# Performance work log

Measured on AMD Instinct MI355X. Metric: run time of the kernel, lower is better.

The kernel has to match this reference:

```python
import jax, jax.numpy as jnp
import numpy as np

H = 128          # hidden_dim
L = 3            # n_layers
G = 128          # num graphs in batch
BN_EPS = 1e-5


def setup_inputs() -> dict:
    key = jax.random.key(0)
    ks = jax.random.split(key, 16)
    N, E, ND, ED = 2048, 8192, 32, 16
    s = lambda k, shape, fan: jax.random.normal(k, shape, dtype=jnp.float32) / np.sqrt(fan)
    return {
        "x": jax.random.normal(ks[0], (N, ND), dtype=jnp.float32),
        "edge_index": jax.random.randint(ks[1], (2, E), 0, N),
        "edge_attr": jax.random.normal(ks[2], (E, ED), dtype=jnp.float32),
        "batch": jnp.sort(jax.random.randint(ks[3], (N,), 0, G)),
        "node_W": s(ks[4], (ND, H), ND),
        "node_b": jnp.zeros((H,), jnp.float32),
        "edge_W": s(ks[5], (L, ED, H * H), ED),
        "edge_b": jnp.zeros((L, H * H), jnp.float32),
        "root_W": s(ks[6], (L, H, H), H),
        "conv_bias": jnp.zeros((L, H), jnp.float32),
        "bn_gamma": jnp.ones((L, H), jnp.float32),
        "bn_beta": jnp.zeros((L, H), jnp.float32),
        "cls_W1": s(ks[7], (H, 64), H),
        "cls_b1": jnp.zeros((64,), jnp.float32),
        "cls_W2": s(ks[8], (64, 1), 64),
        "cls_b2": jnp.zeros((1,), jnp.float32),
    }


def _segment_mean(vals, ids, num_segments):
    ssum = jax.ops.segment_sum(vals, ids, num_segments=num_segments)
    cnt = jax.ops.segment_sum(jnp.ones((vals.shape[0],), vals.dtype), ids,
                              num_segments=num_segments)
    return ssum / jnp.maximum(cnt, 1.0)[:, None]


def reference(x, edge_index, edge_attr, batch, node_W, node_b, edge_W, edge_b,
              root_W, conv_bias, bn_gamma, bn_beta, cls_W1, cls_b1, cls_W2, cls_b2):
    N = x.shape[0]
    src, dst = edge_index[0], edge_index[1]
    h = x @ node_W + node_b                                   # [N, H]
    for l in range(L):
        # edge-conditioned weights: [E, H, H]
        W = (edge_attr @ edge_W[l] + edge_b[l]).reshape(-1, H, H)
        msg = jnp.einsum('ei,eio->eo', h[src], W)             # gather + per-edge matmul
        agg = _segment_mean(msg, dst, N)                      # scatter-mean
        x_new = h @ root_W[l] + agg + conv_bias[l]
        # BatchNorm (batch statistics, training-mode math)
        mu = jnp.mean(x_new, axis=0)
        var = jnp.var(x_new, axis=0)
        x_new = (x_new - mu) * jax.lax.rsqrt(var + BN_EPS) * bn_gamma[l] + bn_beta[l]
        x_new = jax.nn.relu(x_new)                            # dropout omitted (eval)
        h = h + x_new                                         # residual
    g = _segment_mean(h, batch, G)                            # global mean pool [G, H]
    out = jax.nn.relu(g @ cls_W1 + cls_b1) @ cls_W2 + cls_b2  # classifier
    return out.squeeze(-1)                                    # [G]
```

## Files before the change

kernel.cpp:

```cpp
#include <hip/hip_runtime.h>
#include <cstddef>
#include <cstdint>

#define H 128
#define EDIM 16
#define NLAYER 3
#define NSLICE 18
#define WCOLS (NSLICE * H)
#define TM 64
#define TN 64
#define TK 16

typedef unsigned short ushort_t;
typedef unsigned int uint_t;
typedef __attribute__((ext_vector_type(8))) short bf16x8;
typedef __attribute__((ext_vector_type(4))) float f32x4;

__device__ __forceinline__ ushort_t f2bf(float f) {
    uint_t u = __builtin_bit_cast(uint_t, f);
    u += 0x7fffu + ((u >> 16) & 1u);
    return (ushort_t)(u >> 16);
}

__global__ __launch_bounds__(256) void gemm_bsliced(
    const float* __restrict__ A, const float* __restrict__ B,
    const float* __restrict__ bias, float* __restrict__ C,
    ushort_t* __restrict__ Cbf, int M, int K, int N)
{
    __shared__ float As[TK][TM + 4];
    __shared__ float Bs[TK][TN + 4];
    const int bm = blockIdx.y * TM;
    const int bn = blockIdx.x * TN;
    const int tid = threadIdx.x;
    const int tx = tid & 15;
    const int ty = tid >> 4;

    float acc[4][4];
#pragma unroll
    for (int i = 0; i < 4; ++i)
#pragma unroll
        for (int j = 0; j < 4; ++j) acc[i][j] = 0.f;

    const int ka = tid & 15, ma = tid >> 4;
    const int nb = tid & 63, kb = tid >> 6;

    for (int k0 = 0; k0 < K; k0 += TK) {
#pragma unroll
        for (int r = 0; r < 4; ++r)
            As[ka][ma + 16 * r] = A[(size_t)(bm + ma + 16 * r) * K + (k0 + ka)];
#pragma unroll
        for (int r = 0; r < 4; ++r)
            Bs[kb + 4 * r][nb] = B[(size_t)(k0 + kb + 4 * r) * N + bn + nb];
        __syncthreads();
#pragma unroll
        for (int kk = 0; kk < TK; ++kk) {
            const float4 a4 = *(const float4*)&As[kk][ty * 4];
            const float4 b4 = *(const float4*)&Bs[kk][tx * 4];
            const float a[4] = {a4.x, a4.y, a4.z, a4.w};
            const float b[4] = {b4.x, b4.y, b4.z, b4.w};
#pragma unroll
            for (int i = 0; i < 4; ++i)
#pragma unroll
                for (int j = 0; j < 4; ++j)
                    acc[i][j] = fmaf(a[i], b[j], acc[i][j]);
        }
        __syncthreads();
    }

#pragma unroll
    for (int i = 0; i < 4; ++i) {
        const int row = bm + ty * 4 + i;
        float4 v;
        v.x = acc[i][0] + bias[(bn + tx * 4 + 0) & 127];
        v.y = acc[i][1] + bias[(bn + tx * 4 + 1) & 127];
        v.z = acc[i][2] + bias[(bn + tx * 4 + 2) & 127];
        v.w = acc[i][3] + bias[(bn + tx * 4 + 3) & 127];
        *(float4*)&C[(size_t)row * N + bn + tx * 4] = v;
        if (Cbf) {
            ushort_t* o = &Cbf[(size_t)row * N + bn + tx * 4];
            o[0] = f2bf(v.x); o[1] = f2bf(v.y); o[2] = f2bf(v.z); o[3] = f2bf(v.w);
        }
    }
}

__global__ __launch_bounds__(256) void prep_weights(
    const float* __restrict__ eW, const float* __restrict__ eb,
    const float* __restrict__ rW, ushort_t* __restrict__ Wt)
{
    __shared__ ushort_t tile[128][136];
    const int b = blockIdx.x;
    const int l = b / NSLICE, s = b % NSLICE;
    const float* S = (s < 16) ? (eW + ((size_t)l * 16 + s) * (H * H))
                   : (s == 16 ? (eb + (size_t)l * H * H)
                              : (rW + (size_t)l * H * H));
    const int t = threadIdx.x;
    const int k = t >> 1, o0 = (t & 1) * 64;
#pragma unroll
    for (int j = 0; j < 64; j += 4) {
        float4 v = *(const float4*)&S[(size_t)k * H + o0 + j];
        tile[k][o0 + j + 0] = f2bf(v.x);
        tile[k][o0 + j + 1] = f2bf(v.y);
        tile[k][o0 + j + 2] = f2bf(v.z);
        tile[k][o0 + j + 3] = f2bf(v.w);
    }
    __syncthreads();
    const int n = t >> 1, k0 = (t & 1) * 64;
    ushort_t* out = Wt + ((size_t)l * WCOLS + s * H + n) * H + k0;
#pragma unroll 8
    for (int j = 0; j < 64; ++j) out[j] = tile[k0 + j][n];
}

__global__ __launch_bounds__(256) void mfma_gemm(
    const ushort_t* __restrict__ hbf, const ushort_t* __restrict__ Wt,
    float* __restrict__ C)
{
    __shared__ ushort_t As[64][136];
    __shared__ ushort_t Bs[64][136];
    const int tid = threadIdx.x;
    const int v0 = blockIdx.y * 64;
    const int n0 = blockIdx.x * 64;

    {
        const int row = tid >> 2, col0 = (tid & 3) * 32;
        const ushort_t* ga = hbf + (size_t)(v0 + row) * H + col0;
        const ushort_t* gb = Wt + (size_t)(n0 + row) * H + col0;
#pragma unroll
        for (int j = 0; j < 32; j += 8) {
            *(uint4*)&As[row][col0 + j] = *(const uint4*)(ga + j);
            *(uint4*)&Bs[row][col0 + j] = *(const uint4*)(gb + j);
        }
    }
    __syncthreads();

    const int wave = tid >> 6, lane = tid & 63;
    const int l15 = lane & 15, kg = lane >> 4;
    const int mrow = wave * 16 + l15;

    f32x4 acc0 = {0.f, 0.f, 0.f, 0.f};
    f32x4 acc1 = {0.f, 0.f, 0.f, 0.f};
    f32x4 acc2 = {0.f, 0.f, 0.f, 0.f};
    f32x4 acc3 = {0.f, 0.f, 0.f, 0.f};

#pragma unroll
    for (int s = 0; s < 4; ++s) {
        const int k = s * 32 + kg * 8;
        bf16x8 a = *(const bf16x8*)&As[mrow][k];
        bf16x8 b0 = *(const bf16x8*)&Bs[0 * 16 + l15][k];
        bf16x8 b1 = *(const bf16x8*)&Bs[1 * 16 + l15][k];
        bf16x8 b2 = *(const bf16x8*)&Bs[2 * 16 + l15][k];
        bf16x8 b3 = *(const bf16x8*)&Bs[3 * 16 + l15][k];
        acc0 = __builtin_amdgcn_mfma_f32_16x16x32_bf16(a, b0, acc0, 0, 0, 0);
        acc1 = __builtin_amdgcn_mfma_f32_16x16x32_bf16(a, b1, acc1, 0, 0, 0);
        acc2 = __builtin_amdgcn_mfma_f32_16x16x32_bf16(a, b2, acc2, 0, 0, 0);
        acc3 = __builtin_amdgcn_mfma_f32_16x16x32_bf16(a, b3, acc3, 0, 0, 0);
    }

    const size_t base = (size_t)(v0 + wave * 16 + kg * 4) * WCOLS + n0 + l15;
#pragma unroll
    for (int r = 0; r < 4; ++r) {
        C[base + (size_t)r * WCOLS + 0]  = acc0[r];
        C[base + (size_t)r * WCOLS + 16] = acc1[r];
        C[base + (size_t)r * WCOLS + 32] = acc2[r];
        C[base + (size_t)r * WCOLS + 48] = acc3[r];
    }
}

__global__ void count_kernel(const int* __restrict__ dst, const int* __restrict__ batch,
                             float* cntN, float* cntG, int E, int N)
{
    int t = blockIdx.x * 256 + threadIdx.x;
    if (t < E) atomicAdd(&cntN[dst[t]], 1.f);
    if (t < N) atomicAdd(&cntG[batch[t]], 1.f);
}

__global__ __launch_bounds__(256) void edge_combine(
    const float* __restrict__ Pbuf, const float* __restrict__ ea,
    const int* __restrict__ src, const int* __restrict__ dst,
    float* __restrict__ agg, int E)
{
    const int e = blockIdx.x * 2 + (threadIdx.x >> 7);
    const int o = threadIdx.x & 127;
    if (e >= E) return;
    const int s = src[e], d = dst[e];
    const float* Pe = Pbuf + (size_t)s * WCOLS;
    float m = Pe[16 * H + o];
#pragma unroll
    for (int dd = 0; dd < EDIM; ++dd)
        m = fmaf(ea[e * EDIM + dd], Pe[dd * H + o], m);
    atomicAdd(&agg[d * H + o], m);
}

__global__ __launch_bounds__(256) void stats_kernel(
    const float* __restrict__ Pbuf, const float* __restrict__ agg,
    const float* __restrict__ cnt, const float* __restrict__ conv_b,
    float* __restrict__ xnew, float* __restrict__ bnS, float* __restrict__ bnQ)
{
    __shared__ float s1[H], s2[H];
    const int c = threadIdx.x & 127;
    const int half = threadIdx.x >> 7;
    const int row0 = blockIdx.x * 32;
    const float cb = conv_b[c];
    float s = 0.f, q = 0.f;
    for (int r = half; r < 32; r += 2) {
        const int v = row0 + r;
        const float rc = 1.0f / fmaxf(cnt[v], 1.0f);
        const float val = Pbuf[(size_t)v * WCOLS + 17 * H + c] + cb
                        + agg[v * H + c] * rc;
        xnew[v * H + c] = val;
        s += val;
        q += val * val;
    }
    if (half == 1) { s1[c] = s; s2[c] = q; }
    __syncthreads();
    if (half == 0) {
        atomicAdd(&bnS[c], s + s1[c]);
        atomicAdd(&bnQ[c], q + s2[c]);
    }
}

__global__ __launch_bounds__(256) void bn_apply(
    float* __restrict__ h, ushort_t* __restrict__ hbf,
    const float* __restrict__ xnew,
    const float* __restrict__ bnS, const float* __restrict__ bnQ,
    const float* __restrict__ gamma, const float* __restrict__ beta,
    const int* __restrict__ batch, float* __restrict__ gsum, int N, int last)
{
    const int idx = blockIdx.x * 256 + threadIdx.x;
    const int c = idx & 127;
    const int v = idx >> 7;
    const float invN = 1.0f / (float)N;
    const float mu = bnS[c] * invN;
    const float var = bnQ[c] * invN - mu * mu;
    const float val = (xnew[idx] - mu) * rsqrtf(var + 1e-5f) * gamma[c] + beta[c];
    const float hn = h[idx] + fmaxf(val, 0.f);
    h[idx] = hn;
    hbf[idx] = f2bf(hn);
    if (last) atomicAdd(&gsum[batch[v] * H + c], hn);
}

__global__ void classifier_kernel(
    const float* __restrict__ gsum, const float* __restrict__ cntG,
    const float* __restrict__ W1, const float* __restrict__ b1,
    const float* __restrict__ W2, const float* __restrict__ b2,
    float* __restrict__ out)
{
    const int g = blockIdx.x;
    const int j = threadIdx.x;
    const float rc = 1.0f / fmaxf(cntG[g], 1.0f);
    float acc = b1[j];
#pragma unroll 8
    for (int i = 0; i < H; ++i)
        acc = fmaf(gsum[g * H + i] * rc, W1[i * 64 + j], acc);
    float pv = fmaxf(acc, 0.f) * W2[j];
#pragma unroll
    for (int off = 32; off > 0; off >>= 1)
        pv += __shfl_down(pv, off);
    if (j == 0) out[g] = pv + b2[0];
}

extern "C" void kernel_launch(void* const* d_in, const int* in_sizes, int n_in,
                              void* d_out, int out_size, void* d_ws, size_t ws_size,
                              hipStream_t stream)
{
    const float* x      = (const float*)d_in[0];
    const int*   eidx   = (const int*)  d_in[1];
    const float* eattr  = (const float*)d_in[2];
    const int*   batch  = (const int*)  d_in[3];
    const float* node_W = (const float*)d_in[4];
    const float* node_b = (const float*)d_in[5];
    const float* edge_W = (const float*)d_in[6];
    const float* edge_b = (const float*)d_in[7];
    const float* root_W = (const float*)d_in[8];
    const float* conv_b = (const float*)d_in[9];
    const float* gamma  = (const float*)d_in[10];
    const float* beta   = (const float*)d_in[11];
    const float* W1     = (const float*)d_in[12];
    const float* b1     = (const float*)d_in[13];
    const float* W2     = (const float*)d_in[14];
    const float* b2     = (const float*)d_in[15];
    float* out = (float*)d_out;

    const int N = in_sizes[0] / 32;
    const int E = in_sizes[1] / 2;
    const int G = out_size;

    float* ws = (float*)d_ws;
    float* agg  = ws;
    float* cntN = agg  + (size_t)3 * N * H;
    float* cntG = cntN + N;
    float* bnS  = cntG + G;
    float* bnQ  = bnS  + NLAYER * H;
    float* gsum = bnQ  + NLAYER * H;
    float* h    = gsum + (size_t)G * H;
    float* xnew = h    + (size_t)N * H;
    ushort_t* hbf = (ushort_t*)(xnew + (size_t)N * H);
    ushort_t* Wt  = hbf + (size_t)N * H;
    float* Pbuf = (float*)(Wt + (size_t)NLAYER * WCOLS * H);

    const size_t zf = (size_t)3 * N * H + N + G + 2 * NLAYER * H + (size_t)G * H;
    hipMemsetAsync(agg, 0, zf * sizeof(float), stream);

    const int* src = eidx;
    const int* dst = eidx + E;

    const int tmax = (E > N ? E : N);
    count_kernel<<<(tmax + 255) / 256, 256, 0, stream>>>(dst, batch, cntN, cntG, E, N);

    prep_weights<<<NLAYER * NSLICE, 256, 0, stream>>>(edge_W, edge_b, root_W, Wt);

    gemm_bsliced<<<dim3(H / TN, N / TM), 256, 0, stream>>>(
        x, node_W, node_b, h, hbf, N, 32, H);

    for (int l = 0; l < NLAYER; ++l) {
        float* agg_l = agg + (size_t)l * N * H;
        mfma_gemm<<<dim3(WCOLS / 64, N / 64), 256, 0, stream>>>(
            hbf, Wt + (size_t)l * WCOLS * H, Pbuf);
        edge_combine<<<E / 2, 256, 0, stream>>>(Pbuf, eattr, src, dst, agg_l, E);
        stats_kernel<<<N / 32, 256, 0, stream>>>(
            Pbuf, agg_l, cntN, conv_b + (size_t)l * H, xnew, bnS + l * H, bnQ + l * H);
        bn_apply<<<(N * H) / 256, 256, 0, stream>>>(
            h, hbf, xnew, bnS + l * H, bnQ + l * H,
            gamma + (size_t)l * H, beta + (size_t)l * H,
            batch, gsum, N, l == NLAYER - 1);
    }

    classifier_kernel<<<G, 64, 0, stream>>>(gsum, cntG, W1, b1, W2, b2, out);
}
```

Baseline: 208.1 us.

## Replace atomic scatter with CSR gather fused into BN stats; store projections in bf16

Builds a CSR-by-destination edge ordering once (histogram, scan, scatter) so each layer gathers incoming edges per node instead of doing per-edge float atomics into a zeroed aggregate buffer. The edge combine and the batch-norm statistics kernels are fused into one kernel, and the per-node edge projections are written in bf16 to halve the gather traffic. Count and weight-prep kernels are merged into one launch, and the large memset of aggregation buffers goes away. Costs are three small setup kernels (including a single-block scan), uneven per-node work from varying degree, and extra bf16 rounding of the projections.

```diff
diff --git a/kernel.cpp b/kernel.cpp
--- a/kernel.cpp
+++ b/kernel.cpp
@@ -7,6 +7,7 @@
 #define NLAYER 3
 #define NSLICE 18
 #define WCOLS (NSLICE * H)
+#define PCOLS (EDIM * H)
 #define TM 64
 #define TN 64
 #define TK 16
@@ -21,8 +22,85 @@
     u += 0x7fffu + ((u >> 16) & 1u);
     return (ushort_t)(u >> 16);
 }
-
-__global__ __launch_bounds__(256) void gemm_bsliced(
+__device__ __forceinline__ float bf_lo(uint_t u) {
+    return __builtin_bit_cast(float, u << 16);
+}
+__device__ __forceinline__ float bf_hi(uint_t u) {
+    return __builtin_bit_cast(float, u & 0xffff0000u);
+}
+
+__global__ __launch_bounds__(256) void setup_kernel(
+    const int* __restrict__ dst, const int* __restrict__ batch,
+    int* __restrict__ hist, float* __restrict__ cntG, int E, int N,
+    const float* __restrict__ eW, const float* __restrict__ eb,
+    const float* __restrict__ rW, ushort_t* __restrict__ Wt)
+{
+    if (blockIdx.x < 32) {
+        int t = blockIdx.x * 256 + threadIdx.x;
+        if (t < E) atomicAdd(&hist[dst[t]], 1);
+        if (t < N) atomicAdd(&cntG[batch[t]], 1.f);
+        return;
+    }
+    __shared__ ushort_t tile[128][136];
+    const int b = blockIdx.x - 32;
+    const int l = b / NSLICE, s = b % NSLICE;
+    const float* S = (s < 16) ? (eW + ((size_t)l * 16 + s) * (H * H))
+                   : (s == 16 ? (eb + (size_t)l * H * H)
+                              : (rW + (size_t)l * H * H));
+    const int t = threadIdx.x;
+    const int k = t >> 1, o0 = (t & 1) * 64;
+#pragma unroll
+    for (int j = 0; j < 64; j += 4) {
+        float4 v = *(const float4*)&S[(size_t)k * H + o0 + j];
+        tile[k][o0 + j + 0] = f2bf(v.x);
+        tile[k][o0 + j + 1] = f2bf(v.y);
+        tile[k][o0 + j + 2] = f2bf(v.z);
+        tile[k][o0 + j + 3] = f2bf(v.w);
+    }
+    __syncthreads();
+    const int n = t >> 1, k0 = (t & 1) * 64;
+    ushort_t* outp = Wt + ((size_t)l * WCOLS + s * H + n) * H + k0;
+#pragma unroll 8
+    for (int j = 0; j < 64; ++j) outp[j] = tile[k0 + j][n];
+}
+
+__global__ __launch_bounds__(256) void scan_kernel(
+    const int* __restrict__ hist, int* __restrict__ offs, int N)
+{
+    __shared__ int part[256];
+    const int t = threadIdx.x;
+    const int base = t * 8;
+    int v[8], loc[8], s = 0;
+#pragma unroll
+    for (int j = 0; j < 8; ++j) v[j] = hist[base + j];
+#pragma unroll
+    for (int j = 0; j < 8; ++j) { loc[j] = s; s += v[j]; }
+    part[t] = s;
+    __syncthreads();
+    for (int off = 1; off < 256; off <<= 1) {
+        int x = (t >= off) ? part[t - off] : 0;
+        __syncthreads();
+        part[t] += x;
+        __syncthreads();
+    }
+    const int boff = (t == 0) ? 0 : part[t - 1];
+#pragma unroll
+    for (int j = 0; j < 8; ++j) offs[base + j] = boff + loc[j];
+    if (t == 255) offs[N] = boff + s;
+}
+
+__global__ void scatter_kernel(const int* __restrict__ dst,
+                               const int* __restrict__ offs,
+                               int* __restrict__ fill, int* __restrict__ eord, int E)
+{
+    const int e = blockIdx.x * 256 + threadIdx.x;
+    if (e >= E) return;
+    const int d = dst[e];
+    const int pos = offs[d] + atomicAdd(&fill[d], 1);
+    eord[pos] = e;
+}
+
+__global__ __launch_bounds__(256) void gemm_embed(
     const float* __restrict__ A, const float* __restrict__ B,
     const float* __restrict__ bias, float* __restrict__ C,
     ushort_t* __restrict__ Cbf, int M, int K, int N)
@@ -76,43 +154,14 @@
         v.z = acc[i][2] + bias[(bn + tx * 4 + 2) & 127];
         v.w = acc[i][3] + bias[(bn + tx * 4 + 3) & 127];
         *(float4*)&C[(size_t)row * N + bn + tx * 4] = v;
-        if (Cbf) {
-            ushort_t* o = &Cbf[(size_t)row * N + bn + tx * 4];
-            o[0] = f2bf(v.x); o[1] = f2bf(v.y); o[2] = f2bf(v.z); o[3] = f2bf(v.w);
-        }
-    }
-}
-
-__global__ __launch_bounds__(256) void prep_weights(
-    const float* __restrict__ eW, const float* __restrict__ eb,
-    const float* __restrict__ rW, ushort_t* __restrict__ Wt)
-{
-    __shared__ ushort_t tile[128][136];
-    const int b = blockIdx.x;
-    const int l = b / NSLICE, s = b % NSLICE;
-    const float* S = (s < 16) ? (eW + ((size_t)l * 16 + s) * (H * H))
-                   : (s == 16 ? (eb + (size_t)l * H * H)
-                              : (rW + (size_t)l * H * H));
-    const int t = threadIdx.x;
-    const int k = t >> 1, o0 = (t & 1) * 64;
-#pragma unroll
-    for (int j = 0; j < 64; j += 4) {
-        float4 v = *(const float4*)&S[(size_t)k * H + o0 + j];
-        tile[k][o0 + j + 0] = f2bf(v.x);
-        tile[k][o0 + j + 1] = f2bf(v.y);
-        tile[k][o0 + j + 2] = f2bf(v.z);
-        tile[k][o0 + j + 3] = f2bf(v.w);
-    }
-    __syncthreads();
-    const int n = t >> 1, k0 = (t & 1) * 64;
-    ushort_t* out = Wt + ((size_t)l * WCOLS + s * H + n) * H + k0;
-#pragma unroll 8
-    for (int j = 0; j < 64; ++j) out[j] = tile[k0 + j][n];
+        ushort_t* o = &Cbf[(size_t)row * N + bn + tx * 4];
+        o[0] = f2bf(v.x); o[1] = f2bf(v.y); o[2] = f2bf(v.z); o[3] = f2bf(v.w);
+    }
 }
 
 __global__ __launch_bounds__(256) void mfma_gemm(
     const ushort_t* __restrict__ hbf, const ushort_t* __restrict__ Wt,
-    float* __restrict__ C)
+    ushort_t* __restrict__ Pb, float* __restrict__ QR)
 {
     __shared__ ushort_t As[64][136];
     __shared__ ushort_t Bs[64][136];
@@ -155,66 +204,82 @@
         acc3 = __builtin_amdgcn_mfma_f32_16x16x32_bf16(a, b3, acc3, 0, 0, 0);
     }
 
-    const size_t base = (size_t)(v0 + wave * 16 + kg * 4) * WCOLS + n0 + l15;
-#pragma unroll
-    for (int r = 0; r < 4; ++r) {
-        C[base + (size_t)r * WCOLS + 0]  = acc0[r];
-        C[base + (size_t)r * WCOLS + 16] = acc1[r];
-        C[base + (size_t)r * WCOLS + 32] = acc2[r];
-        C[base + (size_t)r * WCOLS + 48] = acc3[r];
-    }
-}
-
-__global__ void count_kernel(const int* __restrict__ dst, const int* __restrict__ batch,
-                             float* cntN, float* cntG, int E, int N)
-{
-    int t = blockIdx.x * 256 + threadIdx.x;
-    if (t < E) atomicAdd(&cntN[dst[t]], 1.f);
-    if (t < N) atomicAdd(&cntG[batch[t]], 1.f);
-}
-
-__global__ __launch_bounds__(256) void edge_combine(
-    const float* __restrict__ Pbuf, const float* __restrict__ ea,
-    const int* __restrict__ src, const int* __restrict__ dst,
-    float* __restrict__ agg, int E)
-{
-    const int e = blockIdx.x * 2 + (threadIdx.x >> 7);
-    const int o = threadIdx.x & 127;
-    if (e >= E) return;
-    const int s = src[e], d = dst[e];
-    const float* Pe = Pbuf + (size_t)s * WCOLS;
-    float m = Pe[16 * H + o];
-#pragma unroll
-    for (int dd = 0; dd < EDIM; ++dd)
-        m = fmaf(ea[e * EDIM + dd], Pe[dd * H + o], m);
-    atomicAdd(&agg[d * H + o], m);
-}
-
-__global__ __launch_bounds__(256) void stats_kernel(
-    const float* __restrict__ Pbuf, const float* __restrict__ agg,
-    const float* __restrict__ cnt, const float* __restrict__ conv_b,
+    const int slice = n0 >> 7;
+    const int lo = n0 & 127;
+    const int row0 = v0 + wave * 16 + kg * 4;
+    if (slice < 16) {
+        ushort_t* op = Pb + (size_t)row0 * PCOLS + slice * H + lo + l15;
+#pragma unroll
+        for (int r = 0; r < 4; ++r) {
+            op[(size_t)r * PCOLS + 0]  = f2bf(acc0[r]);
+            op[(size_t)r * PCOLS + 16] = f2bf(acc1[r]);
+            op[(size_t)r * PCOLS + 32] = f2bf(acc2[r]);
+            op[(size_t)r * PCOLS + 48] = f2bf(acc3[r]);
+        }
+    } else {
+        float* op = QR + (size_t)row0 * 256 + (slice - 16) * H + lo + l15;
+#pragma unroll
+        for (int r = 0; r < 4; ++r) {
+            op[(size_t)r * 256 + 0]  = acc0[r];
+            op[(size_t)r * 256 + 16] = acc1[r];
+            op[(size_t)r * 256 + 32] = acc2[r];
+            op[(size_t)r * 256 + 48] = acc3[r];
+        }
+    }
+}
+
+__global__ __launch_bounds__(256) void edge_stats(
+    const ushort_t* __restrict__ Pb, const float* __restrict__ QR,
+    const float* __restrict__ ea, const int* __restrict__ srcArr,
+    const int* __restrict__ offs, const int* __restrict__ hist,
+    const int* __restrict__ eord, const float* __restrict__ conv_b,
     float* __restrict__ xnew, float* __restrict__ bnS, float* __restrict__ bnQ)
 {
-    __shared__ float s1[H], s2[H];
-    const int c = threadIdx.x & 127;
-    const int half = threadIdx.x >> 7;
-    const int row0 = blockIdx.x * 32;
-    const float cb = conv_b[c];
-    float s = 0.f, q = 0.f;
-    for (int r = half; r < 32; r += 2) {
-        const int v = row0 + r;
-        const float rc = 1.0f / fmaxf(cnt[v], 1.0f);
-        const float val = Pbuf[(size_t)v * WCOLS + 17 * H + c] + cb
-                        + agg[v * H + c] * rc;
-        xnew[v * H + c] = val;
-        s += val;
-        q += val * val;
-    }
-    if (half == 1) { s1[c] = s; s2[c] = q; }
+    __shared__ float sS[4][H];
+    __shared__ float sQ[4][H];
+    const int tid = threadIdx.x;
+    const int sb = tid >> 6;
+    const int o2 = tid & 63;
+    const int v = blockIdx.x * 4 + sb;
+
+    const int st = offs[v];
+    const int deg = hist[v];
+    float m0 = 0.f, m1 = 0.f;
+    for (int k = 0; k < deg; ++k) {
+        const int e = eord[st + k];
+        const int s = srcArr[e];
+        const float* eap = ea + (size_t)e * EDIM;
+        const float4 w0 = *(const float4*)(eap + 0);
+        const float4 w1 = *(const float4*)(eap + 4);
+        const float4 w2 = *(const float4*)(eap + 8);
+        const float4 w3 = *(const float4*)(eap + 12);
+        const float w[16] = {w0.x, w0.y, w0.z, w0.w, w1.x, w1.y, w1.z, w1.w,
+                             w2.x, w2.y, w2.z, w2.w, w3.x, w3.y, w3.z, w3.w};
+        const uint_t* prow = (const uint_t*)(Pb + (size_t)s * PCOLS) + o2;
+        const float2 q2 = *(const float2*)(QR + (size_t)s * 256 + 2 * o2);
+        m0 += q2.x;
+        m1 += q2.y;
+#pragma unroll
+        for (int d = 0; d < EDIM; ++d) {
+            const uint_t u = prow[(size_t)d * 64];
+            m0 = fmaf(w[d], bf_lo(u), m0);
+            m1 = fmaf(w[d], bf_hi(u), m1);
+        }
+    }
+    const float rc = 1.0f / (float)(deg > 0 ? deg : 1);
+    const float2 rt = *(const float2*)(QR + (size_t)v * 256 + H + 2 * o2);
+    const float2 cb = *(const float2*)(conv_b + 2 * o2);
+    const float val0 = m0 * rc + rt.x + cb.x;
+    const float val1 = m1 * rc + rt.y + cb.y;
+    *(float2*)(xnew + (size_t)v * H + 2 * o2) = make_float2(val0, val1);
+    sS[sb][2 * o2] = val0; sS[sb][2 * o2 + 1] = val1;
+    sQ[sb][2 * o2] = val0 * val0; sQ[sb][2 * o2 + 1] = val1 * val1;
     __syncthreads();
-    if (half == 0) {
-        atomicAdd(&bnS[c], s + s1[c]);
-        atomicAdd(&bnQ[c], q + s2[c]);
+    if (tid < H) {
+        const float s4 = sS[0][tid] + sS[1][tid] + sS[2][tid] + sS[3][tid];
+        const float q4 = sQ[0][tid] + sQ[1][tid] + sQ[2][tid] + sQ[3][tid];
+        atomicAdd(&bnS[tid], s4);
+        atomicAdd(&bnQ[tid], q4);
     }
 }
 
@@ -284,40 +349,42 @@
     const int E = in_sizes[1] / 2;
     const int G = out_size;
 
-    float* ws = (float*)d_ws;
-    float* agg  = ws;
-    float* cntN = agg  + (size_t)3 * N * H;
-    float* cntG = cntN + N;
+    int* hist   = (int*)d_ws;
+    int* fill   = hist + N;
+    float* cntG = (float*)(fill + N);
     float* bnS  = cntG + G;
-    float* bnQ  = bnS  + NLAYER * H;
-    float* gsum = bnQ  + NLAYER * H;
-    float* h    = gsum + (size_t)G * H;
-    float* xnew = h    + (size_t)N * H;
+    float* bnQ  = bnS + NLAYER * H;
+    float* gsum = bnQ + NLAYER * H;
+    int* offs   = (int*)(gsum + (size_t)G * H);
+    int* eord   = offs + (N + 16);
+    float* h    = (float*)(eord + E);
+    float* xnew = h + (size_t)N * H;
     ushort_t* hbf = (ushort_t*)(xnew + (size_t)N * H);
     ushort_t* Wt  = hbf + (size_t)N * H;
-    float* Pbuf = (float*)(Wt + (size_t)NLAYER * WCOLS * H);
-
-    const size_t zf = (size_t)3 * N * H + N + G + 2 * NLAYER * H + (size_t)G * H;
-    hipMemsetAsync(agg, 0, zf * sizeof(float), stream);
+    ushort_t* Pb  = Wt + (size_t)NLAYER * WCOLS * H;
+    float* QR   = (float*)(Pb + (size_t)N * PCOLS);
+
+    const size_t zbytes = (size_t)(2 * N) * 4
+                        + ((size_t)G + 2 * NLAYER * H + (size_t)G * H) * 4;
+    hipMemsetAsync(hist, 0, zbytes, stream);
 
     const int* src = eidx;
     const int* dst = eidx + E;
 
-    const int tmax = (E > N ? E : N);
-    count_kernel<<<(tmax + 255) / 256, 256, 0, stream>>>(dst, batch, cntN, cntG, E, N);
-
-    prep_weights<<<NLAYER * NSLICE, 256, 0, stream>>>(edge_W, edge_b, root_W, Wt);
-
-    gemm_bsliced<<<dim3(H / TN, N / TM), 256, 0, stream>>>(
+    setup_kernel<<<32 + NLAYER * NSLICE, 256, 0, stream>>>(
+        dst, batch, hist, cntG, E, N, edge_W, edge_b, root_W, Wt);
+    scan_kernel<<<1, 256, 0, stream>>>(hist, offs, N);
+    scatter_kernel<<<E / 256, 256, 0, stream>>>(dst, offs, fill, eord, E);
+
+    gemm_embed<<<dim3(H / TN, N / TM), 256, 0, stream>>>(
         x, node_W, node_b, h, hbf, N, 32, H);
 
     for (int l = 0; l < NLAYER; ++l) {
-        float* agg_l = agg + (size_t)l * N * H;
         mfma_gemm<<<dim3(WCOLS / 64, N / 64), 256, 0, stream>>>(
-            hbf, Wt + (size_t)l * WCOLS * H, Pbuf);
-        edge_combine<<<E / 2, 256, 0, stream>>>(Pbuf, eattr, src, dst, agg_l, E);
-        stats_kernel<<<N / 32, 256, 0, stream>>>(
-            Pbuf, agg_l, cntN, conv_b + (size_t)l * H, xnew, bnS + l * H, bnQ + l * H);
+            hbf, Wt + (size_t)l * WCOLS * H, Pb, QR);
+        edge_stats<<<N / 4, 256, 0, stream>>>(
+            Pb, QR, eattr, src, offs, hist, eord,
+            conv_b + (size_t)l * H, xnew, bnS + l * H, bnQ + l * H);
         bn_apply<<<(N * H) / 256, 256, 0, stream>>>(
             h, hbf, xnew, bnS + l * H, bnQ + l * H,
             gamma + (size_t)l * H, beta + (size_t)l * H,
```

After: 205.7 us. Within noise of the previous version (-1.1%).
